# Performance work log

Hardware: AMD Instinct MI355X
Metric: run time of the kernel (lower is better)

Reference implementation:

```python
import jax, jax.numpy as jnp
import numpy as np

NUM_CLASSES = 3
SCALE_XY = 1.05
ANCHORS = np.array([[12.0, 16.0, 0.0, 0.0],
                    [19.0, 36.0, 0.0, 0.0],
                    [40.0, 28.0, 0.0, 0.0]], dtype=np.float32)  # (w, h, im, re)
NUM_ANCHORS = ANCHORS.shape[0]


def setup_inputs() -> dict:
    key = jax.random.key(0)
    B, G = 64, 152
    C = NUM_ANCHORS * (NUM_CLASSES + 7)  # 30
    x = jax.random.normal(key, (B, C, G, G), dtype=jnp.float32)
    return {"x": x, "img_size": 1216}


def reference(x, img_size):
    nB, _, _, g = x.shape
    stride = jnp.float32(img_size) / g
    # [B, A, C+7, G, G] -> [B, A, G, G, C+7]
    pred = x.reshape(nB, NUM_ANCHORS, NUM_CLASSES + 7, g, g).transpose(0, 1, 3, 4, 2)

    bx = jax.nn.sigmoid(pred[..., 0]) * SCALE_XY - 0.5 * (SCALE_XY - 1)
    by = jax.nn.sigmoid(pred[..., 1]) * SCALE_XY - 0.5 * (SCALE_XY - 1)
    w = pred[..., 2]
    h = pred[..., 3]
    im = pred[..., 4]
    re = pred[..., 5]
    pred_conf = jax.nn.sigmoid(pred[..., 6])
    pred_cls = jax.nn.sigmoid(pred[..., 7:])

    grid = jnp.arange(g, dtype=jnp.float32)
    grid_x = grid[None, None, None, :]        # broadcasts over rows
    grid_y = grid[None, None, :, None]        # broadcasts over cols
    anchors = jnp.asarray(ANCHORS)
    anchor_w = (anchors[:, 0] / stride)[None, :, None, None]
    anchor_h = (anchors[:, 1] / stride)[None, :, None, None]

    sg = jax.lax.stop_gradient  # original uses .detach() for pred_boxes
    pbx = sg(bx) + grid_x
    pby = sg(by) + grid_y
    pbw = jnp.exp(sg(w)) * anchor_w
    pbh = jnp.exp(sg(h)) * anchor_h
    pbim = sg(im)
    pbre = sg(re)

    N = NUM_ANCHORS * g * g
    boxes_xywh = jnp.stack([pbx, pby, pbw, pbh], axis=-1).reshape(nB, N, 4) * stride
    boxes_imre = jnp.stack([pbim, pbre], axis=-1).reshape(nB, N, 2)
    output = jnp.concatenate(
        [boxes_xywh,
         boxes_imre,
         pred_conf.reshape(nB, N, 1),
         pred_cls.reshape(nB, N, NUM_CLASSES)], axis=-1)
    return output
```

## Files before the change

kernel.cpp:

```cpp
#include <hip/hip_runtime.h>


constexpr int G    = 152;
constexpr int G2   = G * G;
constexpr int NA   = 3;
constexpr int NOUT = 10;
constexpr int P4   = G2 / 4;

__device__ __forceinline__ float fast_sigmoid(float v) {
    return 1.0f / (1.0f + __expf(-v));
}

__global__ __launch_bounds__(256) void yolo_kernel(
    const float* __restrict__ x,
    const int*   __restrict__ img_size_p,
    float*       __restrict__ out,
    int total4)
{
    int idx = blockIdx.x * 256 + threadIdx.x;
    if (idx >= total4) return;

    int iv = *img_size_p;
    float img_size;
    if (iv > 0 && iv < (1 << 20)) {
        img_size = (float)iv;
    } else {
        img_size = __int_as_float(iv);
    }
    const float stride = img_size / (float)G;

    const float aw[NA] = {12.0f, 19.0f, 40.0f};
    const float ah[NA] = {16.0f, 36.0f, 28.0f};

    int pos4 = idx % P4;
    int ba   = idx / P4;
    int a    = ba % NA;

    int pos = pos4 * 4;
    int y   = pos / G;
    int x0  = pos - y * G;

    float4 p[NOUT];
    const float* xbase = x + (size_t)ba * (NOUT * G2) + pos;
#pragma unroll
    for (int ch = 0; ch < NOUT; ++ch)
        p[ch] = *reinterpret_cast<const float4*>(xbase + (size_t)ch * G2);

    const float anchor_w = (aw[a] / stride) * stride;
    const float anchor_h = (ah[a] / stride) * stride;

    alignas(16) float buf[4 * NOUT];
#pragma unroll
    for (int j = 0; j < 4; ++j) {
        const float v0 = reinterpret_cast<const float*>(&p[0])[j];
        const float v1 = reinterpret_cast<const float*>(&p[1])[j];
        const float v2 = reinterpret_cast<const float*>(&p[2])[j];
        const float v3 = reinterpret_cast<const float*>(&p[3])[j];
        const float v4 = reinterpret_cast<const float*>(&p[4])[j];
        const float v5 = reinterpret_cast<const float*>(&p[5])[j];
        const float v6 = reinterpret_cast<const float*>(&p[6])[j];
        const float v7 = reinterpret_cast<const float*>(&p[7])[j];
        const float v8 = reinterpret_cast<const float*>(&p[8])[j];
        const float v9 = reinterpret_cast<const float*>(&p[9])[j];

        const float bx = fast_sigmoid(v0) * 1.05f - 0.5f * (1.05f - 1.0f);
        const float by = fast_sigmoid(v1) * 1.05f - 0.5f * (1.05f - 1.0f);

        buf[j * NOUT + 0] = (bx + (float)(x0 + j)) * stride;
        buf[j * NOUT + 1] = (by + (float)y) * stride;
        buf[j * NOUT + 2] = __expf(v2) * anchor_w;
        buf[j * NOUT + 3] = __expf(v3) * anchor_h;
        buf[j * NOUT + 4] = v4;
        buf[j * NOUT + 5] = v5;
        buf[j * NOUT + 6] = fast_sigmoid(v6);
        buf[j * NOUT + 7] = fast_sigmoid(v7);
        buf[j * NOUT + 8] = fast_sigmoid(v8);
        buf[j * NOUT + 9] = fast_sigmoid(v9);
    }

    float4* op = reinterpret_cast<float4*>(out + (size_t)(ba * G2 + pos) * NOUT);
#pragma unroll
    for (int k = 0; k < NOUT; ++k)
        op[k] = reinterpret_cast<const float4*>(buf)[k];
}

extern "C" void kernel_launch(void* const* d_in, const int* in_sizes, int n_in,
                              void* d_out, int out_size, void* d_ws, size_t ws_size,
                              hipStream_t stream) {
    const float* x = (const float*)d_in[0];
    const int* img_size_p = (const int*)d_in[1];
    float* out = (float*)d_out;

    const int total4 = 64 * NA * P4;
    const int blocks = (total4 + 255) / 256;
    yolo_kernel<<<blocks, 256, 0, stream>>>(x, img_size_p, out, total4);
}
```

Before: 320.2 us.

## Stage outputs through LDS for coalesced nontemporal block stores

Each thread's 40 output floats are written into shared memory, and after a barrier the block writes its contiguous output region with fully coalesced 16-byte nontemporal stores. Previously each thread wrote 160 contiguous bytes on its own, which gave strided wavefront stores. The bounds check is removed on the assumption that the total work divides 256 exactly. This holds here (64*3*5776 = 1108992 = 4332*256). The cost is 40KB of LDS per block, which limits occupancy, plus an extra barrier.

```diff
diff --git a/kernel.cpp b/kernel.cpp
--- a/kernel.cpp
+++ b/kernel.cpp
@@ -7,6 +7,8 @@
 constexpr int NOUT = 10;
 constexpr int P4   = G2 / 4;
 
+typedef float floatx4 __attribute__((ext_vector_type(4)));
+
 __device__ __forceinline__ float fast_sigmoid(float v) {
     return 1.0f / (1.0f + __expf(-v));
 }
@@ -14,31 +16,27 @@
 __global__ __launch_bounds__(256) void yolo_kernel(
     const float* __restrict__ x,
     const int*   __restrict__ img_size_p,
-    float*       __restrict__ out,
-    int total4)
+    float*       __restrict__ out)
 {
-    int idx = blockIdx.x * 256 + threadIdx.x;
-    if (idx >= total4) return;
+    __shared__ float lds[256 * 4 * NOUT];
+
+    const int t   = threadIdx.x;
+    const int idx = blockIdx.x * 256 + t;
 
     int iv = *img_size_p;
-    float img_size;
-    if (iv > 0 && iv < (1 << 20)) {
-        img_size = (float)iv;
-    } else {
-        img_size = __int_as_float(iv);
-    }
+    float img_size = (iv > 0 && iv < (1 << 20)) ? (float)iv : __int_as_float(iv);
     const float stride = img_size / (float)G;
 
     const float aw[NA] = {12.0f, 19.0f, 40.0f};
     const float ah[NA] = {16.0f, 36.0f, 28.0f};
 
-    int pos4 = idx % P4;
-    int ba   = idx / P4;
-    int a    = ba % NA;
+    const int pos4 = idx % P4;
+    const int ba   = idx / P4;
+    const int a    = ba % NA;
 
-    int pos = pos4 * 4;
-    int y   = pos / G;
-    int x0  = pos - y * G;
+    const int pos = pos4 * 4;
+    const int y   = pos / G;
+    const int x0  = pos - y * G;
 
     float4 p[NOUT];
     const float* xbase = x + (size_t)ba * (NOUT * G2) + pos;
@@ -78,10 +76,20 @@
         buf[j * NOUT + 9] = fast_sigmoid(v9);
     }
 
-    float4* op = reinterpret_cast<float4*>(out + (size_t)(ba * G2 + pos) * NOUT);
+    floatx4* l4 = reinterpret_cast<floatx4*>(lds);
+    const floatx4* b4 = reinterpret_cast<const floatx4*>(buf);
 #pragma unroll
-    for (int k = 0; k < NOUT; ++k)
-        op[k] = reinterpret_cast<const float4*>(buf)[k];
+    for (int w = 0; w < NOUT; ++w)
+        l4[t * NOUT + w] = b4[w];
+
+    __syncthreads();
+
+    floatx4* dst = reinterpret_cast<floatx4*>(out) + (size_t)blockIdx.x * (256 * NOUT);
+#pragma unroll
+    for (int r = 0; r < NOUT; ++r) {
+        floatx4 v = l4[r * 256 + t];
+        __builtin_nontemporal_store(v, dst + r * 256 + t);
+    }
 }
 
 extern "C" void kernel_launch(void* const* d_in, const int* in_sizes, int n_in,
@@ -92,6 +100,6 @@
     float* out = (float*)d_out;
 
     const int total4 = 64 * NA * P4;
-    const int blocks = (total4 + 255) / 256;
-    yolo_kernel<<<blocks, 256, 0, stream>>>(x, img_size_p, out, total4);
+    const int blocks = total4 / 256;
+    yolo_kernel<<<blocks, 256, 0, stream>>>(x, img_size_p, out);
 }
```

After: 304.9 us. 1.05x faster.
